# Optimization experiments

Hardware: AMD Instinct MI355X
Metric: run time of the kernel (lower is better)

The kernel has to match this reference:

```python
import jax, jax.numpy as jnp
import numpy as np

B, H, W = 8, 48, 48
D_MODEL, D_STATE, SSM_RATIO, K = 192, 16, 2.0, 4
D_INNER = int(SSM_RATIO * D_MODEL)        # 384
DT_RANK = int(np.ceil(D_MODEL / 16))       # 12
EPS = 1e-6


def setup_inputs() -> dict:
    key = jax.random.key(0)
    ks = jax.random.split(key, 12)
    s = 0.02
    inp = {
        "x": jax.random.normal(ks[0], (B, H, W, D_MODEL), jnp.float32),
        "in_proj_w": s * jax.random.normal(ks[1], (2 * D_INNER, D_MODEL), jnp.float32),
        "conv_w": s * jax.random.normal(ks[2], (D_INNER, 1, 3, 3), jnp.float32),
        "conv_b": jnp.zeros((D_INNER,), jnp.float32),
        "x_proj_w": s * jax.random.normal(ks[3], (K, DT_RANK + 2 * D_STATE, D_INNER), jnp.float32),
        "dt_w": s * jax.random.normal(ks[4], (K, D_INNER, DT_RANK), jnp.float32),
        "dt_bias": 0.05 * jax.random.normal(ks[5], (K, D_INNER), jnp.float32),
        "A_logs": jnp.log(jnp.broadcast_to(jnp.arange(1, D_STATE + 1, dtype=jnp.float32), (K * D_INNER, D_STATE)).copy()),
        "Ds": jnp.ones((K * D_INNER,), jnp.float32),
        "ln_w": jnp.ones((D_INNER,), jnp.float32),
        "ln_b": jnp.zeros((D_INNER,), jnp.float32),
        "out_proj_w": s * jax.random.normal(ks[6], (D_MODEL, D_INNER), jnp.float32),
    }
    return inp


def _selective_scan(u, dt, A, Bs, Cs):
    # u, dt: (B,K,D,L); A: (K,D,N); Bs, Cs: (B,K,N,L)
    u_t = jnp.moveaxis(u, -1, 0)    # (L,B,K,D)
    dt_t = jnp.moveaxis(dt, -1, 0)  # (L,B,K,D)
    B_t = jnp.moveaxis(Bs, -1, 0)   # (L,B,K,N)
    C_t = jnp.moveaxis(Cs, -1, 0)   # (L,B,K,N)
    b = u.shape[0]
    h0 = jnp.zeros((b, K, D_INNER, D_STATE), jnp.float32)

    def step(h, inp):
        ut, dtt, bt, ct = inp
        dA = jnp.exp(dtt[..., None] * A)                       # (B,K,D,N)
        h = dA * h + (dtt * ut)[..., None] * bt[:, :, None, :]  # (B,K,D,N)
        y = jnp.einsum('bkdn,bkn->bkd', h, ct)
        return h, y

    _, ys = jax.lax.scan(step, h0, (u_t, dt_t, B_t, C_t))
    return jnp.moveaxis(ys, 0, -1)  # (B,K,D,L)


def reference(x, in_proj_w, conv_w, conv_b, x_proj_w, dt_w, dt_bias, A_logs, Ds, ln_w, ln_b, out_proj_w):
    b, h, w, _ = x.shape
    L = h * w
    # in_proj + split into x / gate z
    xz = jnp.einsum('bhwc,oc->bhwo', x, in_proj_w)
    xi, z = jnp.split(xz, 2, axis=-1)
    z = jax.nn.silu(z)
    # depthwise 3x3 conv, channel-first
    xi = jnp.transpose(xi, (0, 3, 1, 2))  # (B,Di,H,W)
    xi = jax.lax.conv_general_dilated(
        xi, conv_w, window_strides=(1, 1), padding='SAME',
        feature_group_count=D_INNER,
        dimension_numbers=('NCHW', 'OIHW', 'NCHW')) + conv_b[None, :, None, None]
    xi = jax.nn.silu(xi)
    # cross-scan: 4 directions (row-major, col-major, and their reverses)
    xr = xi.reshape(b, D_INNER, L)
    xc = jnp.transpose(xi, (0, 1, 3, 2)).reshape(b, D_INNER, L)
    xs = jnp.stack([xr, xc, jnp.flip(xr, -1), jnp.flip(xc, -1)], axis=1)  # (B,K,D,L)
    # per-direction projections
    x_dbl = jnp.einsum('bkdl,kcd->bkcl', xs, x_proj_w)  # (B,K,R+2N,L)
    dts = x_dbl[:, :, :DT_RANK]
    Bs = x_dbl[:, :, DT_RANK:DT_RANK + D_STATE]
    Cs = x_dbl[:, :, DT_RANK + D_STATE:]
    dts = jnp.einsum('bkrl,kdr->bkdl', dts, dt_w)
    A = -jnp.exp(A_logs.astype(jnp.float32)).reshape(K, D_INNER, D_STATE)
    dt = jax.nn.softplus(dts + dt_bias[None, :, :, None])
    ys = _selective_scan(xs.astype(jnp.float32), dt, A, Bs.astype(jnp.float32), Cs.astype(jnp.float32))
    ys = ys + Ds.reshape(1, K, D_INNER, 1) * xs  # skip
    # cross-merge (invert each direction, sum)
    def col2row(t):
        return jnp.transpose(t.reshape(b, D_INNER, w, h), (0, 1, 3, 2)).reshape(b, D_INNER, L)
    y = ys[:, 0] + col2row(ys[:, 1]) + jnp.flip(ys[:, 2], -1) + col2row(jnp.flip(ys[:, 3], -1))
    y = jnp.transpose(y.reshape(b, D_INNER, h, w), (0, 2, 3, 1))  # (B,H,W,Di)
    # LayerNorm over channel dim
    mu = y.mean(-1, keepdims=True)
    var = ((y - mu) ** 2).mean(-1, keepdims=True)
    y = (y - mu) / jnp.sqrt(var + EPS) * ln_w + ln_b
    # gate + out_proj
    y = y * z
    out = jnp.einsum('bhwd,od->bhwo', y, out_proj_w)
    return out.astype(x.dtype)
```

## Files before the change

### kernel.cpp

```cpp
#include <hip/hip_runtime.h>

#define BB 8
#define HH 48
#define WW2 48
#define LL 2304
#define CIN 192
#define DI 384
#define NK 4
#define RR 12
#define NS 16
#define CD 44
#define NX 176
#define MM 18432
#define NC 32
#define CL 72

typedef unsigned short u16;
typedef __attribute__((ext_vector_type(8))) short s16x8;
typedef __attribute__((ext_vector_type(4))) float f32x4;

static __device__ __forceinline__ float siluf(float x) { return x / (1.f + __expf(-x)); }

static __device__ __forceinline__ u16 f2bf(float x) {
    unsigned u = __float_as_uint(x);
    return (u16)((u + 0x7FFFu + ((u >> 16) & 1u)) >> 16);
}
static __device__ __forceinline__ float bf2f(u16 h) {
    return __uint_as_float(((unsigned)h) << 16);
}

static __device__ __forceinline__ int posmap(int k, int l) {
    switch (k & 3) {
    case 0: return l;
    case 1: { int w = l / HH; int h = l - w * HH; return h * WW2 + w; }
    case 2: return LL - 1 - l;
    default: { int j = LL - 1 - l; int w = j / HH; int h = j - w * HH; return h * WW2 + w; }
    }
}

__global__ __launch_bounds__(256) void k_cvt2(const float* __restrict__ in,
                                              u16* __restrict__ hi,
                                              u16* __restrict__ lo, int n) {
    int i = (blockIdx.x * 256 + threadIdx.x) * 4;
    if (i >= n) return;
    float4 v = *(const float4*)(in + i);
    u16 h0 = f2bf(v.x), h1 = f2bf(v.y), h2 = f2bf(v.z), h3 = f2bf(v.w);
    hi[i + 0] = h0; hi[i + 1] = h1; hi[i + 2] = h2; hi[i + 3] = h3;
    lo[i + 0] = f2bf(v.x - bf2f(h0));
    lo[i + 1] = f2bf(v.y - bf2f(h1));
    lo[i + 2] = f2bf(v.z - bf2f(h2));
    lo[i + 3] = f2bf(v.w - bf2f(h3));
}

template<int N, int K, int EPI>
__global__ __launch_bounds__(256) void k_gemm(const u16* __restrict__ Ahg,
                                              const u16* __restrict__ Alg,
                                              const u16* __restrict__ Bhg,
                                              const u16* __restrict__ Blg,
                                              float* __restrict__ O1,
                                              float* __restrict__ O2) {
    __shared__ __align__(16) u16 lds[12288];
    const int m0 = blockIdx.x << 7;
    const int n0 = blockIdx.y << 6;
    const int t = threadIdx.x;
    const int lane = t & 63;
    const int w = t >> 6;
    const int wm = w & 1, wn = w >> 1;

    f32x4 acc[4][2];
#pragma unroll
    for (int mi = 0; mi < 4; ++mi)
#pragma unroll
        for (int ni = 0; ni < 2; ++ni)
#pragma unroll
            for (int r = 0; r < 4; ++r) acc[mi][ni][r] = 0.f;

    const int rA = lane & 15;
    const int kb = (lane >> 4) << 3;

    for (int k0 = 0; k0 < K; k0 += 32) {
#pragma unroll
        for (int rep = 0; rep < 2; ++rep) {
            int q = t + (rep << 8);
            int row = q >> 2;
            int kk = (q & 3) << 3;
            size_t ga = (size_t)(m0 + row) * K + k0 + kk;
            *(uint4*)&lds[(row << 5) + kk] = *(const uint4*)(Ahg + ga);
            *(uint4*)&lds[4096 + (row << 5) + kk] = *(const uint4*)(Alg + ga);
        }
        {
            int row = t >> 2;
            int kk = (t & 3) << 3;
            int rg = n0 + row;
            if (N & 63) rg = (rg > N - 1) ? (N - 1) : rg;
            size_t gb = (size_t)rg * K + k0 + kk;
            *(uint4*)&lds[8192 + (row << 5) + kk] = *(const uint4*)(Bhg + gb);
            *(uint4*)&lds[10240 + (row << 5) + kk] = *(const uint4*)(Blg + gb);
        }
        __syncthreads();

        s16x8 bh[2], bl[2];
#pragma unroll
        for (int ni = 0; ni < 2; ++ni) {
            int c = (wn << 5) + (ni << 4) + rA;
            bh[ni] = *(const s16x8*)&lds[8192 + (c << 5) + kb];
            bl[ni] = *(const s16x8*)&lds[10240 + (c << 5) + kb];
        }
#pragma unroll
        for (int mi = 0; mi < 4; ++mi) {
            int rr = (wm << 6) + (mi << 4) + rA;
            s16x8 ah = *(const s16x8*)&lds[(rr << 5) + kb];
            s16x8 al = *(const s16x8*)&lds[4096 + (rr << 5) + kb];
#pragma unroll
            for (int ni = 0; ni < 2; ++ni) {
                acc[mi][ni] = __builtin_amdgcn_mfma_f32_16x16x32_bf16(al, bh[ni], acc[mi][ni], 0, 0, 0);
                acc[mi][ni] = __builtin_amdgcn_mfma_f32_16x16x32_bf16(ah, bl[ni], acc[mi][ni], 0, 0, 0);
                acc[mi][ni] = __builtin_amdgcn_mfma_f32_16x16x32_bf16(ah, bh[ni], acc[mi][ni], 0, 0, 0);
            }
        }
        __syncthreads();
    }

    const int rbase = (lane >> 4) << 2;
#pragma unroll
    for (int mi = 0; mi < 4; ++mi) {
#pragma unroll
        for (int ni = 0; ni < 2; ++ni) {
            int o = n0 + (wn << 5) + (ni << 4) + (lane & 15);
#pragma unroll
            for (int r = 0; r < 4; ++r) {
                int m = m0 + (wm << 6) + (mi << 4) + rbase + r;
                float v = acc[mi][ni][r];
                if (EPI == 0) {
                    if (o < DI) O1[(size_t)m * DI + o] = v;
                    else        O2[(size_t)m * DI + (o - DI)] = siluf(v);
                } else if (EPI == 1) {
                    if (o < NX) O1[(size_t)m * NX + o] = v;
                } else {
                    O1[(size_t)m * CIN + o] = v;
                }
            }
        }
    }
}

__global__ __launch_bounds__(128) void k_conv(const float* __restrict__ xi,
                                              const float* __restrict__ cw,
                                              const float* __restrict__ cb,
                                              float* __restrict__ ub,
                                              u16* __restrict__ ubh,
                                              u16* __restrict__ ubl) {
    int blk = blockIdx.x;
    int b = blk / LL, p = blk - b * LL;
    int h = p / WW2, w = p - h * WW2;
    for (int d = threadIdx.x; d < DI; d += 128) {
        float acc = cb[d];
#pragma unroll
        for (int dh = -1; dh <= 1; ++dh) {
            int hh = h + dh;
            if (hh < 0 || hh >= HH) continue;
#pragma unroll
            for (int dw = -1; dw <= 1; ++dw) {
                int ww = w + dw;
                if (ww < 0 || ww >= WW2) continue;
                acc = fmaf(cw[d * 9 + (dh + 1) * 3 + (dw + 1)],
                           xi[((size_t)b * LL + hh * WW2 + ww) * DI + d], acc);
            }
        }
        float o = siluf(acc);
        size_t idx = ((size_t)b * LL + p) * DI + d;
        ub[idx] = o;
        u16 hh2 = f2bf(o);
        ubh[idx] = hh2;
        ubl[idx] = f2bf(o - bf2f(hh2));
    }
}

static __device__ __forceinline__ void adv_p(int k, int& p, int& hh) {
    if (k == 0) { ++p; }
    else if (k == 2) { --p; }
    else if (k == 1) {
        if (hh == HH - 1) { hh = 0; p -= (LL - 1 - HH); }
        else { ++hh; p += WW2; }
    } else {
        if (hh == 0) { hh = HH - 1; p += (LL - 1 - HH); }
        else { --hh; p -= WW2; }
    }
}

static __device__ __forceinline__ void init_p(int k, int l0, int& p, int& hh) {
    hh = 0;
    if (k == 0) p = l0;
    else if (k == 2) p = LL - 1 - l0;
    else if (k == 1) { int w0 = l0 / HH; hh = l0 - w0 * HH; p = hh * WW2 + w0; }
    else { int j0 = LL - 1 - l0; int w0 = j0 / HH; hh = j0 - w0 * HH; p = hh * WW2 + w0; }
}

__global__ __launch_bounds__(128, 4) void k_scan1(const float* __restrict__ ub,
                                                  const float* __restrict__ xdbl,
                                                  const float* __restrict__ dt_w,
                                                  const float* __restrict__ dt_bias,
                                                  const float* __restrict__ A_logs,
                                                  float* __restrict__ HF,
                                                  float* __restrict__ SD) {
    int blk = blockIdx.x;
    int c = blk % NC;
    int t2 = blk / NC;
    int dblk = t2 % 3;
    int bk = t2 / 3;
    int k = bk & 3, b = bk >> 2;
    int d = (dblk << 7) + threadIdx.x;
    int kd = k * DI + d;

    float dtw[RR];
#pragma unroll
    for (int r = 0; r < RR; ++r) dtw[r] = dt_w[(size_t)kd * RR + r];
    float dtb = dt_bias[kd];
    float a[NS];
    bool fast = true;
#pragma unroll
    for (int n = 0; n < NS; ++n) {
        a[n] = -__expf(A_logs[(size_t)kd * NS + n]);
        fast = fast && (fabsf(a[n] + (float)(n + 1)) < 1e-3f * (float)(n + 1));
    }
    int use_fast = __all((int)fast);

    float h[NS];
#pragma unroll
    for (int n = 0; n < NS; ++n) h[n] = 0.f;
    float sumdt = 0.f;

    const float* cb0 = xdbl + (size_t)b * LL * NX + k * CD;
    const float* ubase = ub + (size_t)b * LL * DI + d;
    const int l0 = c * CL;
    int p, hh;
    init_p(k, l0, p, hh);

    if (use_fast) {
        for (int li = 0; li < CL; ++li) {
            const float4* cp4 = (const float4*)(cb0 + (size_t)p * NX);
            float dq[12];
            *(float4*)(dq + 0) = cp4[0];
            *(float4*)(dq + 4) = cp4[1];
            *(float4*)(dq + 8) = cp4[2];
            float s = dtb;
#pragma unroll
            for (int r = 0; r < RR; ++r) s = fmaf(dtw[r], dq[r], s);
            float es = __expf(s);
            float dt = (s > 15.f) ? s : __logf(1.f + es);
            float E = __builtin_amdgcn_rcpf(1.f + es);
            sumdt += dt;
            float uv = ubase[(size_t)p * DI];
            float du = dt * uv;
            float bb2[16];
            *(float4*)(bb2 + 0)  = cp4[3];
            *(float4*)(bb2 + 4)  = cp4[4];
            *(float4*)(bb2 + 8)  = cp4[5];
            *(float4*)(bb2 + 12) = cp4[6];
            float pw = 1.f;
#pragma unroll
            for (int n = 0; n < NS; ++n) {
                pw *= E;
                h[n] = fmaf(du, bb2[n], pw * h[n]);
            }
            adv_p(k, p, hh);
        }
    } else {
        for (int li = 0; li < CL; ++li) {
            int l = l0 + li;
            int pp = posmap(k, l);
            const float* cp = cb0 + (size_t)pp * NX;
            float s = dtb;
#pragma unroll
            for (int r = 0; r < RR; ++r) s = fmaf(dtw[r], cp[r], s);
            float dt = (s > 15.f) ? s : log1pf(__expf(s));
            sumdt += dt;
            float uv = ubase[(size_t)pp * DI];
            float du = dt * uv;
#pragma unroll
            for (int n = 0; n < NS; ++n) {
                float dA = __expf(dt * a[n]);
                h[n] = fmaf(du, cp[RR + n], dA * h[n]);
            }
        }
    }
    size_t base = ((size_t)bk * NC + c);
#pragma unroll
    for (int n = 0; n < NS; ++n) HF[(base * NS + n) * DI + d] = h[n];
    SD[base * DI + d] = sumdt;
}

__global__ __launch_bounds__(256) void k_scan2(const float* __restrict__ A_logs,
                                               float* __restrict__ HF,
                                               const float* __restrict__ SD) {
    int idx = blockIdx.x * 256 + threadIdx.x;
    int bk = idx / DI;
    int d = idx - bk * DI;
    int k = bk & 3;
    int kd = k * DI + d;

    float a[NS];
    bool fast = true;
#pragma unroll
    for (int n = 0; n < NS; ++n) {
        a[n] = -__expf(A_logs[(size_t)kd * NS + n]);
        fast = fast && (fabsf(a[n] + (float)(n + 1)) < 1e-3f * (float)(n + 1));
    }
    int use_fast = __all((int)fast);

    float H[NS];
#pragma unroll
    for (int n = 0; n < NS; ++n) H[n] = 0.f;

    for (int c = 0; c < NC; ++c) {
        size_t base = ((size_t)bk * NC + c);
        float sd = SD[base * DI + d];
        if (use_fast) {
            float E = __expf(-sd);
            float pw = 1.f;
#pragma unroll
            for (int n = 0; n < NS; ++n) {
                pw *= E;
                float hf = HF[(base * NS + n) * DI + d];
                HF[(base * NS + n) * DI + d] = H[n];
                H[n] = fmaf(pw, H[n], hf);
            }
        } else {
#pragma unroll
            for (int n = 0; n < NS; ++n) {
                float dec = __expf(a[n] * sd);
                float hf = HF[(base * NS + n) * DI + d];
                HF[(base * NS + n) * DI + d] = H[n];
                H[n] = fmaf(dec, H[n], hf);
            }
        }
    }
}

__global__ __launch_bounds__(128, 4) void k_scan3(const float* __restrict__ ub,
                                                  const float* __restrict__ xdbl,
                                                  const float* __restrict__ dt_w,
                                                  const float* __restrict__ dt_bias,
                                                  const float* __restrict__ A_logs,
                                                  const float* __restrict__ Ds,
                                                  const float* __restrict__ HF,
                                                  float* __restrict__ ycomb) {
    int blk = blockIdx.x;
    int c = blk % NC;
    int t2 = blk / NC;
    int dblk = t2 % 3;
    int bk = t2 / 3;
    int k = bk & 3, b = bk >> 2;
    int d = (dblk << 7) + threadIdx.x;
    int kd = k * DI + d;

    float dtw[RR];
#pragma unroll
    for (int r = 0; r < RR; ++r) dtw[r] = dt_w[(size_t)kd * RR + r];
    float dtb = dt_bias[kd];
    float dsv = Ds[kd];
    float a[NS];
    bool fast = true;
#pragma unroll
    for (int n = 0; n < NS; ++n) {
        a[n] = -__expf(A_logs[(size_t)kd * NS + n]);
        fast = fast && (fabsf(a[n] + (float)(n + 1)) < 1e-3f * (float)(n + 1));
    }
    int use_fast = __all((int)fast);

    float h[NS];
    size_t sbase = ((size_t)bk * NC + c);
#pragma unroll
    for (int n = 0; n < NS; ++n) h[n] = HF[(sbase * NS + n) * DI + d];

    const float* cb0 = xdbl + (size_t)b * LL * NX + k * CD;
    const float* ubase = ub + (size_t)b * LL * DI + d;
    float* ybase = ycomb + (size_t)b * LL * DI + d;
    const int l0 = c * CL;
    int p, hh;
    init_p(k, l0, p, hh);

    if (use_fast) {
        for (int li = 0; li < CL; ++li) {
            const float4* cp4 = (const float4*)(cb0 + (size_t)p * NX);
            float dq[12];
            *(float4*)(dq + 0) = cp4[0];
            *(float4*)(dq + 4) = cp4[1];
            *(float4*)(dq + 8) = cp4[2];
            float s = dtb;
#pragma unroll
            for (int r = 0; r < RR; ++r) s = fmaf(dtw[r], dq[r], s);
            float es = __expf(s);
            float dt = (s > 15.f) ? s : __logf(1.f + es);
            float E = __builtin_amdgcn_rcpf(1.f + es);
            float uv = ubase[(size_t)p * DI];
            float du = dt * uv;
            float bc[32];
            *(float4*)(bc + 0)  = cp4[3];
            *(float4*)(bc + 4)  = cp4[4];
            *(float4*)(bc + 8)  = cp4[5];
            *(float4*)(bc + 12) = cp4[6];
            *(float4*)(bc + 16) = cp4[7];
            *(float4*)(bc + 20) = cp4[8];
            *(float4*)(bc + 24) = cp4[9];
            *(float4*)(bc + 28) = cp4[10];
            float pw = 1.f, y = 0.f;
#pragma unroll
            for (int n = 0; n < NS; ++n) {
                pw *= E;
                h[n] = fmaf(du, bc[n], pw * h[n]);
                y = fmaf(h[n], bc[NS + n], y);
            }
            atomicAdd(ybase + (size_t)p * DI, fmaf(dsv, uv, y));
            adv_p(k, p, hh);
        }
    } else {
        for (int li = 0; li < CL; ++li) {
            int l = l0 + li;
            int pp = posmap(k, l);
            const float* cp = cb0 + (size_t)pp * NX;
            float s = dtb;
#pragma unroll
            for (int r = 0; r < RR; ++r) s = fmaf(dtw[r], cp[r], s);
            float dt = (s > 15.f) ? s : log1pf(__expf(s));
            float uv = ubase[(size_t)pp * DI];
            float du = dt * uv;
            float y = 0.f;
#pragma unroll
            for (int n = 0; n < NS; ++n) {
                float dA = __expf(dt * a[n]);
                h[n] = fmaf(du, cp[RR + n], dA * h[n]);
                y = fmaf(h[n], cp[RR + NS + n], y);
            }
            atomicAdd(ybase + (size_t)pp * DI, fmaf(dsv, uv, y));
        }
    }
}

static __device__ __forceinline__ float waveRedSum(float v) {
#pragma unroll
    for (int o = 32; o; o >>= 1) v += __shfl_down(v, o);
    return v;
}

__global__ __launch_bounds__(128) void k_lngate(const float* __restrict__ ycomb,
                                                const float* __restrict__ zb,
                                                const float* __restrict__ lnw,
                                                const float* __restrict__ lnb,
                                                u16* __restrict__ ylnh,
                                                u16* __restrict__ ylnl) {
    int m = blockIdx.x;
    const float* yr = ycomb + (size_t)m * DI;
    float v[3];
    float s1 = 0.f, s2 = 0.f;
#pragma unroll
    for (int i = 0; i < 3; ++i) {
        v[i] = yr[threadIdx.x + (i << 7)];
        s1 += v[i];
        s2 = fmaf(v[i], v[i], s2);
    }
    s1 = waveRedSum(s1);
    s2 = waveRedSum(s2);
    __shared__ float p1[2], p2[2];
    int wid = threadIdx.x >> 6, lane = threadIdx.x & 63;
    if (lane == 0) { p1[wid] = s1; p2[wid] = s2; }
    __syncthreads();
    float S1 = p1[0] + p1[1];
    float S2 = p2[0] + p2[1];
    float mu = S1 * (1.f / DI);
    float var = S2 * (1.f / DI) - mu * mu;
    float rstd = rsqrtf(var + 1e-6f);
#pragma unroll
    for (int i = 0; i < 3; ++i) {
        int dd = threadIdx.x + (i << 7);
        float o = ((v[i] - mu) * rstd) * lnw[dd] + lnb[dd];
        float g = o * zb[(size_t)m * DI + dd];
        u16 hh = f2bf(g);
        ylnh[(size_t)m * DI + dd] = hh;
        ylnl[(size_t)m * DI + dd] = f2bf(g - bf2f(hh));
    }
}

extern "C" void kernel_launch(void* const* d_in, const int* in_sizes, int n_in,
                              void* d_out, int out_size, void* d_ws, size_t ws_size,
                              hipStream_t stream) {
    const float* x         = (const float*)d_in[0];
    const float* in_proj_w = (const float*)d_in[1];
    const float* conv_w    = (const float*)d_in[2];
    const float* conv_b    = (const float*)d_in[3];
    const float* x_proj_w  = (const float*)d_in[4];
    const float* dt_w      = (const float*)d_in[5];
    const float* dt_bias   = (const float*)d_in[6];
    const float* A_logs    = (const float*)d_in[7];
    const float* Ds        = (const float*)d_in[8];
    const float* ln_w      = (const float*)d_in[9];
    const float* ln_b      = (const float*)d_in[10];
    const float* out_proj_w= (const float*)d_in[11];
    float* out = (float*)d_out;
    float* ws  = (float*)d_ws;

    const size_t SZ = (size_t)MM * DI;
    float* xi    = ws;
    float* zb    = ws + SZ;
    float* ub    = ws + 2 * SZ;
    float* xdbl  = ws + 3 * SZ;
    float* ycomb = ws + 3 * SZ + (size_t)MM * NX;
    u16*   wpl   = (u16*)(ycomb + SZ);

    u16* wphi  = wpl;
    u16* wplo  = wpl + 147456;
    u16* xpwhi = wpl + 294912;
    u16* xpwlo = wpl + 362496;
    u16* wohi  = wpl + 430080;
    u16* wolo  = wpl + 503808;

    u16* xhi  = (u16*)ub;  u16* xlo  = xhi + (size_t)MM * CIN;
    u16* ubh  = (u16*)ycomb; u16* ubl = ubh + SZ;
    u16* ylnh = (u16*)xi;  u16* ylnl = ylnh + SZ;
    float* HF = xi;
    float* SD = xi + (size_t)BB * NK * NC * NS * DI;

    k_cvt2<<<3456, 256, 0, stream>>>(x, xhi, xlo, MM * CIN);
    k_cvt2<<<144, 256, 0, stream>>>(in_proj_w, wphi, wplo, 768 * CIN);
    k_cvt2<<<66, 256, 0, stream>>>(x_proj_w, xpwhi, xpwlo, NX * DI);
    k_cvt2<<<72, 256, 0, stream>>>(out_proj_w, wohi, wolo, CIN * DI);

    k_gemm<768, CIN, 0><<<dim3(MM / 128, 12), 256, 0, stream>>>(xhi, xlo, wphi, wplo, xi, zb);

    k_conv<<<MM, 128, 0, stream>>>(xi, conv_w, conv_b, ub, ubh, ubl);

    k_gemm<NX, DI, 1><<<dim3(MM / 128, 3), 256, 0, stream>>>(ubh, ubl, xpwhi, xpwlo, xdbl, nullptr);

    hipMemsetAsync(ycomb, 0, SZ * sizeof(float), stream);

    const int nscan = BB * NK * 3 * NC;
    k_scan1<<<nscan, 128, 0, stream>>>(ub, xdbl, dt_w, dt_bias, A_logs, HF, SD);
    k_scan2<<<BB * NK * DI / 256, 256, 0, stream>>>(A_logs, HF, SD);
    k_scan3<<<nscan, 128, 0, stream>>>(ub, xdbl, dt_w, dt_bias, A_logs, Ds, HF, ycomb);

    k_lngate<<<MM, 128, 0, stream>>>(ycomb, zb, ln_w, ln_b, ylnh, ylnl);

    k_gemm<CIN, DI, 2><<<dim3(MM / 128, 3), 256, 0, stream>>>(ylnh, ylnl, wohi, wolo, out, nullptr);
}
```

Before: 384.7 us.

## Use packed FP32 math and double-buffered row prefetch in scan kernels

Rewrites the fast paths of the chunked scan kernels (pass 1 and pass 3) to use v_pk_fma/v_pk_mul/v_pk_add on pairs of state elements, halving the VALU instruction count for the recurrence and output dot product. The time loop is unrolled by two with register double-buffering, so the next timestep's B/C/dt row and u value are loaded while the current step computes, hiding global-load latency. It also makes the position advance branchless and drops the occupancy hint from launch_bounds. The risk is higher register pressure from two full row buffers (up to 88 floats in scan3), which could lower occupancy or cause spills.

```diff
diff --git a/kernel.cpp b/kernel.cpp
--- a/kernel.cpp
+++ b/kernel.cpp
@@ -18,6 +18,7 @@
 typedef unsigned short u16;
 typedef __attribute__((ext_vector_type(8))) short s16x8;
 typedef __attribute__((ext_vector_type(4))) float f32x4;
+typedef __attribute__((ext_vector_type(2))) float f32x2;
 
 static __device__ __forceinline__ float siluf(float x) { return x / (1.f + __expf(-x)); }
 
@@ -28,6 +29,18 @@
 static __device__ __forceinline__ float bf2f(u16 h) {
     return __uint_as_float(((unsigned)h) << 16);
 }
+
+static __device__ __forceinline__ f32x2 pk_fma(f32x2 a, f32x2 b, f32x2 c) {
+    f32x2 d; asm("v_pk_fma_f32 %0, %1, %2, %3" : "=v"(d) : "v"(a), "v"(b), "v"(c)); return d;
+}
+static __device__ __forceinline__ f32x2 pk_mul(f32x2 a, f32x2 b) {
+    f32x2 d; asm("v_pk_mul_f32 %0, %1, %2" : "=v"(d) : "v"(a), "v"(b)); return d;
+}
+static __device__ __forceinline__ f32x2 pk_add(f32x2 a, f32x2 b) {
+    f32x2 d; asm("v_pk_add_f32 %0, %1, %2" : "=v"(d) : "v"(a), "v"(b)); return d;
+}
+static __device__ __forceinline__ f32x2 pxy(f32x4 v) { f32x2 r; r[0] = v[0]; r[1] = v[1]; return r; }
+static __device__ __forceinline__ f32x2 pzw(f32x4 v) { f32x2 r; r[0] = v[2]; r[1] = v[3]; return r; }
 
 static __device__ __forceinline__ int posmap(int k, int l) {
     switch (k & 3) {
@@ -180,11 +193,13 @@
     if (k == 0) { ++p; }
     else if (k == 2) { --p; }
     else if (k == 1) {
-        if (hh == HH - 1) { hh = 0; p -= (LL - 1 - HH); }
-        else { ++hh; p += WW2; }
+        bool wrap = (hh == HH - 1);
+        hh = wrap ? 0 : hh + 1;
+        p += wrap ? -(LL - 1 - HH) : WW2;
     } else {
-        if (hh == 0) { hh = HH - 1; p += (LL - 1 - HH); }
-        else { --hh; p -= WW2; }
+        bool wrap = (hh == 0);
+        hh = wrap ? HH - 1 : hh - 1;
+        p += wrap ? (LL - 1 - HH) : -WW2;
     }
 }
 
@@ -196,13 +211,26 @@
     else { int j0 = LL - 1 - l0; int w0 = j0 / HH; hh = j0 - w0 * HH; p = hh * WW2 + w0; }
 }
 
-__global__ __launch_bounds__(128, 4) void k_scan1(const float* __restrict__ ub,
-                                                  const float* __restrict__ xdbl,
-                                                  const float* __restrict__ dt_w,
-                                                  const float* __restrict__ dt_bias,
-                                                  const float* __restrict__ A_logs,
-                                                  float* __restrict__ HF,
-                                                  float* __restrict__ SD) {
+#define BPAIR(RW, i) ((i & 1) ? pzw(RW[3 + ((i) >> 1)]) : pxy(RW[3 + ((i) >> 1)]))
+#define CPAIR(RW, i) ((i & 1) ? pzw(RW[7 + ((i) >> 1)]) : pxy(RW[7 + ((i) >> 1)]))
+
+#define DT_HEAD(RW)                                                          \
+    f32x2 cA = pk_mul(dtw2[0], pxy(RW[0])); cA = pk_fma(dtw2[3], pzw(RW[1]), cA); \
+    f32x2 cB = pk_mul(dtw2[1], pzw(RW[0])); cB = pk_fma(dtw2[4], pxy(RW[2]), cB); \
+    f32x2 cC = pk_mul(dtw2[2], pxy(RW[1])); cC = pk_fma(dtw2[5], pzw(RW[2]), cC); \
+    cA = pk_add(cA, cB); cA = pk_add(cA, cC);                                \
+    float s = dtb + cA[0] + cA[1];                                           \
+    float es = __expf(s); float f1 = 1.f + es;                               \
+    float dtv = (s > 15.f) ? s : __logf(f1);                                 \
+    float E = __builtin_amdgcn_rcpf(f1);
+
+__global__ __launch_bounds__(128) void k_scan1(const float* __restrict__ ub,
+                                               const float* __restrict__ xdbl,
+                                               const float* __restrict__ dt_w,
+                                               const float* __restrict__ dt_bias,
+                                               const float* __restrict__ A_logs,
+                                               float* __restrict__ HF,
+                                               float* __restrict__ SD) {
     int blk = blockIdx.x;
     int c = blk % NC;
     int t2 = blk / NC;
@@ -212,9 +240,12 @@
     int d = (dblk << 7) + threadIdx.x;
     int kd = k * DI + d;
 
-    float dtw[RR];
-#pragma unroll
-    for (int r = 0; r < RR; ++r) dtw[r] = dt_w[(size_t)kd * RR + r];
+    f32x2 dtw2[6];
+#pragma unroll
+    for (int r = 0; r < 6; ++r) {
+        dtw2[r][0] = dt_w[(size_t)kd * RR + 2 * r];
+        dtw2[r][1] = dt_w[(size_t)kd * RR + 2 * r + 1];
+    }
     float dtb = dt_bias[kd];
     float a[NS];
     bool fast = true;
@@ -225,46 +256,65 @@
     }
     int use_fast = __all((int)fast);
 
-    float h[NS];
-#pragma unroll
-    for (int n = 0; n < NS; ++n) h[n] = 0.f;
     float sumdt = 0.f;
-
     const float* cb0 = xdbl + (size_t)b * LL * NX + k * CD;
     const float* ubase = ub + (size_t)b * LL * DI + d;
     const int l0 = c * CL;
-    int p, hh;
-    init_p(k, l0, p, hh);
+
+    f32x2 h2[8];
+#pragma unroll
+    for (int i = 0; i < 8; ++i) { h2[i][0] = 0.f; h2[i][1] = 0.f; }
 
     if (use_fast) {
-        for (int li = 0; li < CL; ++li) {
-            const float4* cp4 = (const float4*)(cb0 + (size_t)p * NX);
-            float dq[12];
-            *(float4*)(dq + 0) = cp4[0];
-            *(float4*)(dq + 4) = cp4[1];
-            *(float4*)(dq + 8) = cp4[2];
-            float s = dtb;
-#pragma unroll
-            for (int r = 0; r < RR; ++r) s = fmaf(dtw[r], dq[r], s);
-            float es = __expf(s);
-            float dt = (s > 15.f) ? s : __logf(1.f + es);
-            float E = __builtin_amdgcn_rcpf(1.f + es);
-            sumdt += dt;
-            float uv = ubase[(size_t)p * DI];
-            float du = dt * uv;
-            float bb2[16];
-            *(float4*)(bb2 + 0)  = cp4[3];
-            *(float4*)(bb2 + 4)  = cp4[4];
-            *(float4*)(bb2 + 8)  = cp4[5];
-            *(float4*)(bb2 + 12) = cp4[6];
-            float pw = 1.f;
-#pragma unroll
-            for (int n = 0; n < NS; ++n) {
-                pw *= E;
-                h[n] = fmaf(du, bb2[n], pw * h[n]);
-            }
+#define S1_STEP(RW, UV) do {                                                 \
+        DT_HEAD(RW)                                                          \
+        sumdt += dtv;                                                        \
+        float du = dtv * (UV);                                               \
+        f32x2 du2; du2[0] = du; du2[1] = du;                                 \
+        float ee = E * E;                                                    \
+        f32x2 pw2; pw2[0] = E; pw2[1] = ee;                                  \
+        f32x2 ee2; ee2[0] = ee; ee2[1] = ee;                                 \
+        _Pragma("unroll")                                                    \
+        for (int i = 0; i < 8; ++i) {                                        \
+            f32x2 t = pk_mul(du2, BPAIR(RW, i));                             \
+            h2[i] = pk_fma(pw2, h2[i], t);                                   \
+            if (i < 7) pw2 = pk_mul(pw2, ee2);                               \
+        }                                                                    \
+    } while (0)
+
+        f32x4 ra[7], rb[7];
+        float uva, uvb;
+        int p, hh;
+        init_p(k, l0, p, hh);
+        int pa = p;
+        {
+            const f32x4* c4 = (const f32x4*)(cb0 + (long)pa * NX);
+#pragma unroll
+            for (int i = 0; i < 7; ++i) ra[i] = c4[i];
+            uva = ubase[(long)pa * DI];
+        }
+        adv_p(k, p, hh);
+        for (int li = 0; li < CL; li += 2) {
+            int pb = p;
+            {
+                const f32x4* c4 = (const f32x4*)(cb0 + (long)pb * NX);
+#pragma unroll
+                for (int i = 0; i < 7; ++i) rb[i] = c4[i];
+                uvb = ubase[(long)pb * DI];
+            }
+            S1_STEP(ra, uva);
             adv_p(k, p, hh);
-        }
+            pa = p;
+            {
+                const f32x4* c4 = (const f32x4*)(cb0 + (long)pa * NX);
+#pragma unroll
+                for (int i = 0; i < 7; ++i) ra[i] = c4[i];
+                uva = ubase[(long)pa * DI];
+            }
+            S1_STEP(rb, uvb);
+            adv_p(k, p, hh);
+        }
+#undef S1_STEP
     } else {
         for (int li = 0; li < CL; ++li) {
             int l = l0 + li;
@@ -272,7 +322,7 @@
             const float* cp = cb0 + (size_t)pp * NX;
             float s = dtb;
 #pragma unroll
-            for (int r = 0; r < RR; ++r) s = fmaf(dtw[r], cp[r], s);
+            for (int r = 0; r < 6; ++r) { s = fmaf(dtw2[r][0], cp[2 * r], s); s = fmaf(dtw2[r][1], cp[2 * r + 1], s); }
             float dt = (s > 15.f) ? s : log1pf(__expf(s));
             sumdt += dt;
             float uv = ubase[(size_t)pp * DI];
@@ -280,13 +330,18 @@
 #pragma unroll
             for (int n = 0; n < NS; ++n) {
                 float dA = __expf(dt * a[n]);
-                h[n] = fmaf(du, cp[RR + n], dA * h[n]);
+                float hv = (n & 1) ? h2[n >> 1][1] : h2[n >> 1][0];
+                hv = fmaf(du, cp[RR + n], dA * hv);
+                if (n & 1) h2[n >> 1][1] = hv; else h2[n >> 1][0] = hv;
             }
         }
     }
     size_t base = ((size_t)bk * NC + c);
 #pragma unroll
-    for (int n = 0; n < NS; ++n) HF[(base * NS + n) * DI + d] = h[n];
+    for (int i = 0; i < 8; ++i) {
+        HF[(base * NS + 2 * i) * DI + d] = h2[i][0];
+        HF[(base * NS + 2 * i + 1) * DI + d] = h2[i][1];
+    }
     SD[base * DI + d] = sumdt;
 }
 
@@ -337,14 +392,14 @@
     }
 }
 
-__global__ __launch_bounds__(128, 4) void k_scan3(const float* __restrict__ ub,
-                                                  const float* __restrict__ xdbl,
-                                                  const float* __restrict__ dt_w,
-                                                  const float* __restrict__ dt_bias,
-                                                  const float* __restrict__ A_logs,
-                                                  const float* __restrict__ Ds,
-                                                  const float* __restrict__ HF,
-                                                  float* __restrict__ ycomb) {
+__global__ __launch_bounds__(128) void k_scan3(const float* __restrict__ ub,
+                                               const float* __restrict__ xdbl,
+                                               const float* __restrict__ dt_w,
+                                               const float* __restrict__ dt_bias,
+                                               const float* __restrict__ A_logs,
+                                               const float* __restrict__ Ds,
+                                               const float* __restrict__ HF,
+                                               float* __restrict__ ycomb) {
     int blk = blockIdx.x;
     int c = blk % NC;
     int t2 = blk / NC;
@@ -354,9 +409,12 @@
     int d = (dblk << 7) + threadIdx.x;
     int kd = k * DI + d;
 
-    float dtw[RR];
-#pragma unroll
-    for (int r = 0; r < RR; ++r) dtw[r] = dt_w[(size_t)kd * RR + r];
+    f32x2 dtw2[6];
+#pragma unroll
+    for (int r = 0; r < 6; ++r) {
+        dtw2[r][0] = dt_w[(size_t)kd * RR + 2 * r];
+        dtw2[r][1] = dt_w[(size_t)kd * RR + 2 * r + 1];
+    }
     float dtb = dt_bias[kd];
     float dsv = Ds[kd];
     float a[NS];
@@ -368,52 +426,71 @@
     }
     int use_fast = __all((int)fast);
 
-    float h[NS];
     size_t sbase = ((size_t)bk * NC + c);
-#pragma unroll
-    for (int n = 0; n < NS; ++n) h[n] = HF[(sbase * NS + n) * DI + d];
+    f32x2 h2[8];
+#pragma unroll
+    for (int i = 0; i < 8; ++i) {
+        h2[i][0] = HF[(sbase * NS + 2 * i) * DI + d];
+        h2[i][1] = HF[(sbase * NS + 2 * i + 1) * DI + d];
+    }
 
     const float* cb0 = xdbl + (size_t)b * LL * NX + k * CD;
     const float* ubase = ub + (size_t)b * LL * DI + d;
     float* ybase = ycomb + (size_t)b * LL * DI + d;
     const int l0 = c * CL;
-    int p, hh;
-    init_p(k, l0, p, hh);
 
     if (use_fast) {
-        for (int li = 0; li < CL; ++li) {
-            const float4* cp4 = (const float4*)(cb0 + (size_t)p * NX);
-            float dq[12];
-            *(float4*)(dq + 0) = cp4[0];
-            *(float4*)(dq + 4) = cp4[1];
-            *(float4*)(dq + 8) = cp4[2];
-            float s = dtb;
-#pragma unroll
-            for (int r = 0; r < RR; ++r) s = fmaf(dtw[r], dq[r], s);
-            float es = __expf(s);
-            float dt = (s > 15.f) ? s : __logf(1.f + es);
-            float E = __builtin_amdgcn_rcpf(1.f + es);
-            float uv = ubase[(size_t)p * DI];
-            float du = dt * uv;
-            float bc[32];
-            *(float4*)(bc + 0)  = cp4[3];
-            *(float4*)(bc + 4)  = cp4[4];
-            *(float4*)(bc + 8)  = cp4[5];
-            *(float4*)(bc + 12) = cp4[6];
-            *(float4*)(bc + 16) = cp4[7];
-            *(float4*)(bc + 20) = cp4[8];
-            *(float4*)(bc + 24) = cp4[9];
-            *(float4*)(bc + 28) = cp4[10];
-            float pw = 1.f, y = 0.f;
-#pragma unroll
-            for (int n = 0; n < NS; ++n) {
-                pw *= E;
-                h[n] = fmaf(du, bc[n], pw * h[n]);
-                y = fmaf(h[n], bc[NS + n], y);
-            }
-            atomicAdd(ybase + (size_t)p * DI, fmaf(dsv, uv, y));
+#define S3_STEP(RW, PP, UV) do {                                             \
+        DT_HEAD(RW)                                                          \
+        float du = dtv * (UV);                                               \
+        f32x2 du2; du2[0] = du; du2[1] = du;                                 \
+        float ee = E * E;                                                    \
+        f32x2 pw2; pw2[0] = E; pw2[1] = ee;                                  \
+        f32x2 ee2; ee2[0] = ee; ee2[1] = ee;                                 \
+        f32x2 y2; y2[0] = 0.f; y2[1] = 0.f;                                  \
+        _Pragma("unroll")                                                    \
+        for (int i = 0; i < 8; ++i) {                                        \
+            f32x2 t = pk_mul(du2, BPAIR(RW, i));                             \
+            h2[i] = pk_fma(pw2, h2[i], t);                                   \
+            y2 = pk_fma(h2[i], CPAIR(RW, i), y2);                            \
+            if (i < 7) pw2 = pk_mul(pw2, ee2);                               \
+        }                                                                    \
+        atomicAdd(ybase + (long)(PP) * DI, fmaf(dsv, (UV), y2[0] + y2[1]));  \
+    } while (0)
+
+        f32x4 ra[11], rb[11];
+        float uva, uvb;
+        int p, hh;
+        init_p(k, l0, p, hh);
+        int pa = p;
+        {
+            const f32x4* c4 = (const f32x4*)(cb0 + (long)pa * NX);
+#pragma unroll
+            for (int i = 0; i < 11; ++i) ra[i] = c4[i];
+            uva = ubase[(long)pa * DI];
+        }
+        adv_p(k, p, hh);
+        for (int li = 0; li < CL; li += 2) {
+            int pb = p;
+            {
+                const f32x4* c4 = (const f32x4*)(cb0 + (long)pb * NX);
+#pragma unroll
+                for (int i = 0; i < 11; ++i) rb[i] = c4[i];
+                uvb = ubase[(long)pb * DI];
+            }
+            S3_STEP(ra, pa, uva);
             adv_p(k, p, hh);
-        }
+            pa = p;
+            {
+                const f32x4* c4 = (const f32x4*)(cb0 + (long)pa * NX);
+#pragma unroll
+                for (int i = 0; i < 11; ++i) ra[i] = c4[i];
+                uva = ubase[(long)pa * DI];
+            }
+            S3_STEP(rb, pb, uvb);
+            adv_p(k, p, hh);
+        }
+#undef S3_STEP
     } else {
         for (int li = 0; li < CL; ++li) {
             int l = l0 + li;
@@ -421,7 +498,7 @@
             const float* cp = cb0 + (size_t)pp * NX;
             float s = dtb;
 #pragma unroll
-            for (int r = 0; r < RR; ++r) s = fmaf(dtw[r], cp[r], s);
+            for (int r = 0; r < 6; ++r) { s = fmaf(dtw2[r][0], cp[2 * r], s); s = fmaf(dtw2[r][1], cp[2 * r + 1], s); }
             float dt = (s > 15.f) ? s : log1pf(__expf(s));
             float uv = ubase[(size_t)pp * DI];
             float du = dt * uv;
@@ -429,8 +506,10 @@
 #pragma unroll
             for (int n = 0; n < NS; ++n) {
                 float dA = __expf(dt * a[n]);
-                h[n] = fmaf(du, cp[RR + n], dA * h[n]);
-                y = fmaf(h[n], cp[RR + NS + n], y);
+                float hv = (n & 1) ? h2[n >> 1][1] : h2[n >> 1][0];
+                hv = fmaf(du, cp[RR + n], dA * hv);
+                if (n & 1) h2[n >> 1][1] = hv; else h2[n >> 1][0] = hv;
+                y = fmaf(hv, cp[RR + NS + n], y);
             }
             atomicAdd(ybase + (size_t)pp * DI, fmaf(dsv, uv, y));
         }
```

New measurement: 404.9 us. 5.3% more time.
